# Kernel tuning notes

Hardware: AMD Instinct MI355X
Metric: run time of the kernel (lower is better)

The kernel has to match this reference:

```python
import jax, jax.numpy as jnp
import numpy as np

B, L, HS = 32, 128, 512
P, M = 12, 1024
V, D = 50000, 128
P_TOTAL = 16
CHAR_LEN, CHAR_V = 16, 100
PRI_POS = (0, 1, 2, 3)  # privacy POS tags
TEMP = 1.0              # eval-mode temperature


def setup_inputs() -> dict:
    key = jax.random.key(0)
    ks = jax.random.split(key, 16)
    return {
        "ctx": jax.random.normal(ks[0], (B, L, HS), jnp.float32),
        "dec_W": jax.random.normal(ks[1], (P, HS, M), jnp.float32) * 0.05,
        "dec_b": jax.random.normal(ks[2], (P, M), jnp.float32) * 0.05,
        "psr_weight": jax.random.normal(ks[3], (V, D), jnp.float32),
        "atk_weight": jax.random.normal(ks[4], (V, D), jnp.float32),
        "cpy_W1": jax.random.normal(ks[5], (HS, 64), jnp.float32) * 0.05,
        "cpy_b1": jax.random.normal(ks[6], (64,), jnp.float32) * 0.05,
        "cpy_W2": jax.random.normal(ks[7], (64, 2), jnp.float32) * 0.05,
        "cpy_b2": jax.random.normal(ks[8], (2,), jnp.float32) * 0.05,
        "inp_word": jax.random.randint(ks[9], (B, L), 0, V),
        "inp_pos": jax.random.randint(ks[10], (B, L), 0, P_TOTAL),
        "inp_mask": jnp.ones((B, L), jnp.int32),
        "words": jax.random.randint(ks[11], (P, M), 0, V),
        "lut": jax.random.randint(ks[12], (V, CHAR_LEN), 0, CHAR_V),
    }


def _gumbel_softmax_hard(logits, key, t):
    # hard (straight-through) gumbel-softmax; forward value is one-hot
    u = jax.random.uniform(key, logits.shape, logits.dtype, 1e-6, 1.0 - 1e-6)
    g = -jnp.log(-jnp.log(u))
    y = jax.nn.softmax((logits + g) / t, axis=-1)
    idx = jnp.argmax(y, axis=-1)
    y_hard = jax.nn.one_hot(idx, logits.shape[-1], dtype=y.dtype)
    return y_hard + y - jax.lax.stop_gradient(y), idx


def reference(ctx, dec_W, dec_b, psr_weight, atk_weight,
              cpy_W1, cpy_b1, cpy_W2, cpy_b2,
              inp_word, inp_pos, inp_mask, words, lut):
    bs, ls = inp_word.shape
    N = bs * ls
    gkey = jax.random.key(42)

    ctx_f = ctx.reshape(N, -1)                      # [N, HS]
    pos_f = inp_pos.reshape(N)
    word_f = inp_word.reshape(N)

    ori_psr = psr_weight[word_f]                    # [N, D] gather
    ori_atk = atk_weight[word_f]
    obf_word = word_f
    obf_psr = ori_psr
    obf_atk = ori_atk
    obf_mask = jnp.zeros((N,), bool)
    pri_mask = jnp.zeros((N,), bool)
    entropy = jnp.float32(0.0)

    for p in range(P):  # small fixed set of POS tags (structurally distinct decoders)
        m = pos_f == p                              # [N] routing mask
        obf_mask = obf_mask | m
        if p in PRI_POS:
            pri_mask = pri_mask | m
        cnt = jnp.sum(m.astype(jnp.int32))
        logp = jax.nn.log_softmax(ctx_f @ dec_W[p] + dec_b[p], axis=-1)  # [N, M]
        ent_elem = -logp * jnp.exp(logp)
        ent_p = jnp.sum(jnp.where(m[:, None], ent_elem, 0.0)) / jnp.maximum(cnt * M, 1).astype(jnp.float32)
        entropy = entropy + jnp.where(cnt > 0, ent_p, 0.0)
        spt, idx = _gumbel_softmax_hard(logp, jax.random.fold_in(gkey, p), TEMP)
        spt_word = words[p][idx]                    # map local id -> vocab id
        obf_word = jnp.where(m, spt_word, obf_word)
        psr_p = spt @ psr_weight[words[p]]          # [N, D], per-POS sub-table
        atk_p = spt @ atk_weight[words[p]]
        obf_psr = jnp.where(m[:, None], psr_p, obf_psr)
        obf_atk = jnp.where(m[:, None], atk_p, obf_atk)

    # copy classifier
    h = jax.nn.relu(ctx_f @ cpy_W1 + cpy_b1)
    pcpy = jax.nn.log_softmax(h @ cpy_W2 + cpy_b2, axis=-1)  # [N, 2]
    # do_not_copy_pri: force pcpy to [0, 1] on privacy tokens
    pcpy = jnp.where(pri_mask[:, None], jnp.array([0.0, 1.0], pcpy.dtype), pcpy)

    cpy, _ = _gumbel_softmax_hard(pcpy, jax.random.fold_in(gkey, 999), TEMP)  # [N, 2]
    mask_f = inp_mask.reshape(N).astype(bool)
    cpy_mask = (cpy[:, 0] == 1.0) & mask_f

    noroot = inp_mask.astype(bool).at[:, 0].set(False).reshape(N)
    nr_cnt = jnp.maximum(jnp.sum(noroot.astype(jnp.int32)), 1).astype(jnp.float32)
    logp2 = jax.nn.log_softmax(pcpy, axis=-1)       # F.cross_entropy applies log_softmax again
    cpy_loss = -jnp.sum(jnp.where(noroot, logp2[:, 1], 0.0)) / nr_cnt  # cpy_penalty = 1.0 (applied twice)

    # use_copy: blend original vs obfuscated via (hard) copy gate
    c0, c1 = cpy[:, 0:1], cpy[:, 1:2]
    psr_out = (ori_psr * c0 + obf_psr * c1).reshape(bs, ls, -1)
    atk_out = (ori_atk * c0 + obf_atk * c1).reshape(bs, ls, -1)
    obf_mask = obf_mask & ~cpy_mask
    out_word = (word_f.astype(jnp.float32) * cpy[:, 0]
                + obf_word.astype(jnp.float32) * cpy[:, 1]).astype(jnp.int32).reshape(bs, ls)

    obf_char = lut[out_word]                        # [B, L, CHAR_LEN]
    ent_loss = -entropy  # ent_penalty = 1.0

    return (out_word, obf_char, psr_out, atk_out,
            obf_mask.reshape(bs, ls), cpy_mask.reshape(bs, ls),
            pri_mask.reshape(bs, ls), cpy_loss, ent_loss)
```

## Files before the change

kernel.cpp:

```cpp
#include <hip/hip_runtime.h>
#include <math.h>

#define BB 32
#define LL 128
#define HSZ 512
#define PP 12
#define MM 1024
#define VV 50000
#define DD 128
#define CLEN 16
#define NTOT 4096
#define LISTCAP 512

#define RT 64
#define CT 64
#define BK3 32
#define CPB 16

#define OFF_WORD  0
#define OFF_CHAR  4096
#define OFF_PSR   69632
#define OFF_ATK   593920
#define OFF_OBFM  1118208
#define OFF_CPYM  1122304
#define OFF_PRIM  1126400
#define OFF_CLOSS 1130496
#define OFF_ELOSS 1130497

#define WS_SC_OFF     6656
#define WS_LOGITS_OFF 16384

__device__ __forceinline__ float EXP32(float x){ return (float)exp((double)x); }
__device__ __forceinline__ float LOG32(float x){ return (float)log((double)x); }

__device__ __forceinline__ unsigned rotl32(unsigned x, int r){ return (x<<r)|(x>>(32-r)); }
__device__ __forceinline__ void tf2x32(unsigned k0, unsigned k1, unsigned x0, unsigned x1,
                                       unsigned &o0, unsigned &o1){
  unsigned ks2 = k0 ^ k1 ^ 0x1BD11BDAu;
  x0 += k0; x1 += k1;
  x0+=x1; x1=rotl32(x1,13); x1^=x0;
  x0+=x1; x1=rotl32(x1,15); x1^=x0;
  x0+=x1; x1=rotl32(x1,26); x1^=x0;
  x0+=x1; x1=rotl32(x1, 6); x1^=x0;
  x0+=k1; x1+=ks2+1u;
  x0+=x1; x1=rotl32(x1,17); x1^=x0;
  x0+=x1; x1=rotl32(x1,29); x1^=x0;
  x0+=x1; x1=rotl32(x1,16); x1^=x0;
  x0+=x1; x1=rotl32(x1,24); x1^=x0;
  x0+=ks2; x1+=k0+2u;
  x0+=x1; x1=rotl32(x1,13); x1^=x0;
  x0+=x1; x1=rotl32(x1,15); x1^=x0;
  x0+=x1; x1=rotl32(x1,26); x1^=x0;
  x0+=x1; x1=rotl32(x1, 6); x1^=x0;
  x0+=k0; x1+=k1+3u;
  x0+=x1; x1=rotl32(x1,17); x1^=x0;
  x0+=x1; x1=rotl32(x1,29); x1^=x0;
  x0+=x1; x1=rotl32(x1,16); x1^=x0;
  x0+=x1; x1=rotl32(x1,24); x1^=x0;
  x0+=k1; x1+=ks2+4u;
  x0+=x1; x1=rotl32(x1,13); x1^=x0;
  x0+=x1; x1=rotl32(x1,15); x1^=x0;
  x0+=x1; x1=rotl32(x1,26); x1^=x0;
  x0+=x1; x1=rotl32(x1, 6); x1^=x0;
  x0+=ks2; x1+=k0+5u;
  o0=x0; o1=x1;
}

__device__ __forceinline__ unsigned tf_bits32(unsigned k0, unsigned k1, unsigned e){
  unsigned o0, o1; tf2x32(k0, k1, 0u, e, o0, o1); return o0 ^ o1;
}

__device__ __forceinline__ float bits_to_unif(unsigned bits){
  const float lo = 1e-6f;
  const float hi = (float)(1.0 - 1e-6);
  const float span = hi - lo;
  unsigned fb = (bits >> 9) | 0x3f800000u;
  float f = __fsub_rn(__uint_as_float(fb), 1.0f);
  float r = __fadd_rn(__fmul_rn(f, span), lo);
  return fmaxf(lo, r);
}

__device__ __forceinline__ float gumbel_exact(unsigned bits){
  float u = bits_to_unif(bits);
  float v = -LOG32(u);
  return -LOG32(v);
}
__device__ __forceinline__ float gumbel_fast(unsigned bits){
  float u = bits_to_unif(bits);
  float v = -logf(u);
  return -logf(v);
}

__device__ __forceinline__ void gate_chain(int n, int pos, int msk,
                                           float p0f, float p1f,
                                           const float* __restrict__ cb2,
                                           float* __restrict__ sc0,
                                           float* __restrict__ sc1,
                                           float* __restrict__ closs)
{
  const bool ispri = (pos < 4);
  float pc0 = __fadd_rn(p0f, cb2[0]);
  float pc1 = __fadd_rn(p1f, cb2[1]);
  float m2  = fmaxf(pc0, pc1);
  float s0  = __fsub_rn(pc0, m2), s1 = __fsub_rn(pc1, m2);
  float se  = __fadd_rn(EXP32(s0), EXP32(s1));
  float lse = LOG32(se);
  float q0  = __fsub_rn(s0, lse), q1 = __fsub_rn(s1, lse);
  if (ispri){ q0 = 0.0f; q1 = 1.0f; }

  unsigned k90, k91; tf2x32(0u, 42u, 0u, 999u, k90, k91);
  float g0 = gumbel_exact(tf_bits32(k90, k91, (unsigned)(2*n)));
  float g1 = gumbel_exact(tf_bits32(k90, k91, (unsigned)(2*n + 1)));

  float x0 = __fadd_rn(q0, g0), x1 = __fadd_rn(q1, g1);
  float mmv = fmaxf(x0, x1);
  float ex0 = EXP32(__fsub_rn(x0, mmv));
  float ex1 = EXP32(__fsub_rn(x1, mmv));
  float ssum = __fadd_rn(ex0, ex1);
  float y0 = __fdiv_rn(ex0, ssum), y1 = __fdiv_rn(ex1, ssum);
  int   idx2 = (y1 > y0) ? 1 : 0;
  float ysel = idx2 ? y1 : y0;
  float c    = __fsub_rn(__fadd_rn(1.0f, ysel), ysel);
  *sc0 = (idx2 == 0) ? c : 0.0f;
  *sc1 = (idx2 == 1) ? c : 0.0f;

  float m3 = fmaxf(q0, q1);
  float t0 = __fsub_rn(q0, m3), t1 = __fsub_rn(q1, m3);
  float se2 = __fadd_rn(EXP32(t0), EXP32(t1));
  float l21 = __fsub_rn(t1, LOG32(se2));
  if (msk != 0 && (n & (LL-1)) != 0) atomicAdd(closs, l21);
}

__global__ __launch_bounds__(256)
void cpy_build_kernel(const float* __restrict__ ctx, const float* __restrict__ cW1,
                      const float* __restrict__ cb1, const float* __restrict__ cW2,
                      const float* __restrict__ cb2, const int* __restrict__ inp_pos,
                      const int* __restrict__ inp_mask, int* __restrict__ cntg,
                      int* __restrict__ rowlist, float* __restrict__ scbuf,
                      float* __restrict__ ws)
{
  const int n0 = blockIdx.x * CPB;
  const int t = threadIdx.x;

  if (t < CPB){
    int n = n0 + t;
    int p = inp_pos[n];
    if (p < PP){
      int slot = atomicAdd(&cntg[p], 1);
      if (slot < LISTCAP) rowlist[p*LISTCAP + slot] = n;
    }
  }

  __shared__ float W1s[64][68];
  __shared__ float Cs[CPB][68];

  const int r  = t >> 4;
  const int og = (t & 15) * 4;
  double acc[4] = {0.0, 0.0, 0.0, 0.0};

  for (int k0 = 0; k0 < HSZ; k0 += 64){
    #pragma unroll
    for (int i = 0; i < 4; ++i){
      int s = t + i*256;
      int kk = s >> 4, q = s & 15;
      float4 v = *(const float4*)(cW1 + (size_t)(k0+kk)*64 + q*4);
      *(float4*)&W1s[kk][q*4] = v;
    }
    {
      int rr = t >> 4, q = t & 15;
      float4 v = *(const float4*)(ctx + (size_t)(n0+rr)*HSZ + k0 + q*4);
      *(float4*)&Cs[rr][q*4] = v;
    }
    __syncthreads();
    #pragma unroll 4
    for (int kk = 0; kk < 64; ++kk){
      double c = (double)Cs[r][kk];
      acc[0] += c * (double)W1s[kk][og+0];
      acc[1] += c * (double)W1s[kk][og+1];
      acc[2] += c * (double)W1s[kk][og+2];
      acc[3] += c * (double)W1s[kk][og+3];
    }
    __syncthreads();
  }

  double p0 = 0.0, p1 = 0.0;
  #pragma unroll
  for (int j = 0; j < 4; ++j){
    float hv = __fadd_rn((float)acc[j], cb1[og+j]);
    hv = hv > 0.f ? hv : 0.f;
    double hd = (double)hv;
    p0 += hd * (double)cW2[2*(og+j)+0];
    p1 += hd * (double)cW2[2*(og+j)+1];
  }
  #pragma unroll
  for (int off = 1; off < 16; off <<= 1){
    p0 += __shfl_xor(p0, off);
    p1 += __shfl_xor(p1, off);
  }

  if ((t & 15) == 0){
    const int n = n0 + r;
    float c0v, c1v;
    gate_chain(n, inp_pos[n], inp_mask[n], (float)p0, (float)p1, cb2,
               &c0v, &c1v, ws + 12);
    scbuf[2*n + 0] = c0v;
    scbuf[2*n + 1] = c1v;
  }
}

__global__ __launch_bounds__(256)
void gemm_kernel(const float* __restrict__ ctx, const float* __restrict__ dec_W,
                 const int* __restrict__ cntg, const int* __restrict__ rowlist,
                 float* __restrict__ logits)
{
  const int p  = blockIdx.z;
  const int c0 = blockIdx.x * CT;
  const int r0 = blockIdx.y * RT;
  const int cnt0 = cntg[p];
  const int cnt  = cnt0 < LISTCAP ? cnt0 : LISTCAP;
  if (r0 >= cnt) return;
  const int t = threadIdx.x;

  __shared__ float AsT[BK3][RT+4];
  __shared__ float Bs[BK3][CT+4];
  __shared__ int   rid_s[RT];

  if (t < RT){
    int rr = r0 + t;
    rid_s[t] = rowlist[p*LISTCAP + (rr < cnt ? rr : cnt-1)];
  }
  __syncthreads();

  const int tr = t >> 4, tc = t & 15;
  const int srow = t & 63;
  const int sq   = t >> 6;
  const float* arow = ctx + (size_t)rid_s[srow] * HSZ;

  double acc[4][4];
  #pragma unroll
  for (int i = 0; i < 4; ++i)
    #pragma unroll
    for (int j = 0; j < 4; ++j) acc[i][j] = 0.0;

  const float* Wp = dec_W + (size_t)p * HSZ * MM;

  for (int k0 = 0; k0 < HSZ; k0 += BK3){
    #pragma unroll
    for (int i = 0; i < 2; ++i){
      int kq = sq + i*4;
      float4 v = *(const float4*)(arow + k0 + kq*4);
      AsT[kq*4+0][srow] = v.x;
      AsT[kq*4+1][srow] = v.y;
      AsT[kq*4+2][srow] = v.z;
      AsT[kq*4+3][srow] = v.w;
    }
    #pragma unroll
    for (int i = 0; i < 2; ++i){
      int s = t + i*256;
      int kk = s >> 4, q = s & 15;
      float4 v = *(const float4*)(Wp + (size_t)(k0+kk)*MM + c0 + q*4);
      *(float4*)&Bs[kk][q*4] = v;
    }
    __syncthreads();
    #pragma unroll 4
    for (int kk = 0; kk < BK3; ++kk){
      float4 af = *(const float4*)&AsT[kk][tr*4];
      float4 bf = *(const float4*)&Bs[kk][tc*4];
      double b0=(double)bf.x, b1=(double)bf.y, b2=(double)bf.z, b3=(double)bf.w;
      double a0=(double)af.x, a1=(double)af.y, a2=(double)af.z, a3=(double)af.w;
      acc[0][0]+=a0*b0; acc[0][1]+=a0*b1; acc[0][2]+=a0*b2; acc[0][3]+=a0*b3;
      acc[1][0]+=a1*b0; acc[1][1]+=a1*b1; acc[1][2]+=a1*b2; acc[1][3]+=a1*b3;
      acc[2][0]+=a2*b0; acc[2][1]+=a2*b1; acc[2][2]+=a2*b2; acc[2][3]+=a2*b3;
      acc[3][0]+=a3*b0; acc[3][1]+=a3*b1; acc[3][2]+=a3*b2; acc[3][3]+=a3*b3;
    }
    __syncthreads();
  }

  #pragma unroll
  for (int i = 0; i < 4; ++i){
    int rr = r0 + tr*4 + i;
    if (rr < cnt){
      int rg = rid_s[tr*4 + i];
      float4 o;
      o.x=(float)acc[i][0]; o.y=(float)acc[i][1]; o.z=(float)acc[i][2]; o.w=(float)acc[i][3];
      *(float4*)(logits + (size_t)rg*MM + c0 + tc*4) = o;
    }
  }
}

__global__ __launch_bounds__(256)
void finalize_kernel(const float* __restrict__ dec_b,
                     const float* __restrict__ psr_w, const float* __restrict__ atk_w,
                     const int* __restrict__ inp_word, const int* __restrict__ inp_pos,
                     const int* __restrict__ inp_mask, const int* __restrict__ words,
                     const int* __restrict__ lut, const float* __restrict__ logitsbuf,
                     const float* __restrict__ scbuf,
                     float* __restrict__ out, float* __restrict__ ws)
{
  const int wid = threadIdx.x >> 6, lane = threadIdx.x & 63;
  const int n = blockIdx.x * 4 + wid;

  const int  pos   = inp_pos[n];
  const int  word  = inp_word[n];
  const int  msk   = inp_mask[n];
  const bool isobf = (pos < PP);
  const bool ispri = (pos < 4);
  const float c0 = scbuf[2*n + 0];
  const float c1 = scbuf[2*n + 1];

  int bi = 0;
  if (isobf){
    float l[16];
    float lm = -3.4e38f;
    #pragma unroll
    for (int it = 0; it < 4; ++it){
      int m = it*256 + lane*4;
      float4 lg = *(const float4*)(logitsbuf + (size_t)n*MM + m);
      float4 bq = *(const float4*)(dec_b + (size_t)pos*MM + m);
      l[it*4+0] = __fadd_rn(lg.x, bq.x);
      l[it*4+1] = __fadd_rn(lg.y, bq.y);
      l[it*4+2] = __fadd_rn(lg.z, bq.z);
      l[it*4+3] = __fadd_rn(lg.w, bq.w);
      lm = fmaxf(lm, fmaxf(fmaxf(l[it*4+0], l[it*4+1]), fmaxf(l[it*4+2], l[it*4+3])));
    }
    #pragma unroll
    for (int off = 32; off > 0; off >>= 1) lm = fmaxf(lm, __shfl_xor(lm, off));
    const float xmax = lm;

    float e[16];
    double ds = 0.0;
    #pragma unroll
    for (int j = 0; j < 16; ++j){
      e[j] = expf(__fsub_rn(l[j], xmax));
      ds += (double)e[j];
    }
    #pragma unroll
    for (int off = 32; off > 0; off >>= 1) ds += __shfl_xor(ds, off);
    const double se = ds;
    const float lse = logf((float)se);
    const double inv_se = 1.0 / se;

    unsigned kp0, kp1; tf2x32(0u, 42u, 0u, (unsigned)pos, kp0, kp1);
    float best = -3.4e38f; double es = 0.0;
    #pragma unroll
    for (int it = 0; it < 4; ++it){
      #pragma unroll
      for (int j = 0; j < 4; ++j){
        int m = it*256 + lane*4 + j;
        float sh = __fsub_rn(l[it*4+j], xmax);
        float lp = __fsub_rn(sh, lse);
        es += (double)(-lp) * ((double)e[it*4+j] * inv_se);
        float g = gumbel_fast(tf_bits32(kp0, kp1, (unsigned)(n*MM + m)));
        float sv = __fadd_rn(lp, g);
        if (sv > best){ best = sv; bi = m; }
      }
    }
    #pragma unroll
    for (int off = 32; off > 0; off >>= 1){
      float ov = __shfl_xor(best, off);
      int   oi = __shfl_xor(bi,   off);
      if (ov > best || (ov == best && oi < bi)){ best = ov; bi = oi; }
      es += __shfl_xor(es, off);
    }
    if (lane == 0) atomicAdd(ws + pos, (float)es);
  }

  const int obf_word = isobf ? words[pos*MM + bi] : word;
  float of = __fadd_rn(__fmul_rn((float)word, c0), __fmul_rn((float)obf_word, c1));
  int ow = (int)of;
  if (lane == 0){
    out[OFF_WORD + n] = (float)ow;
    bool cpym = (c0 == 1.0f) && (msk != 0);
    out[OFF_CPYM + n] = cpym ? 1.f : 0.f;
    out[OFF_OBFM + n] = (isobf && !cpym) ? 1.f : 0.f;
    out[OFF_PRIM + n] = ispri ? 1.f : 0.f;
  }
  if (lane < CLEN)
    out[OFF_CHAR + (size_t)n*CLEN + lane] = (float)lut[(size_t)ow*CLEN + lane];
  #pragma unroll
  for (int rep = 0; rep < 2; ++rep){
    int j = lane + rep*64;
    float po = psr_w[(size_t)word*DD + j];
    float pb = isobf ? psr_w[(size_t)obf_word*DD + j] : po;
    out[OFF_PSR + (size_t)n*DD + j] = __fadd_rn(__fmul_rn(po, c0), __fmul_rn(pb, c1));
    float ao = atk_w[(size_t)word*DD + j];
    float ab = isobf ? atk_w[(size_t)obf_word*DD + j] : ao;
    out[OFF_ATK + (size_t)n*DD + j] = __fadd_rn(__fmul_rn(ao, c0), __fmul_rn(ab, c1));
  }
}

__global__ __launch_bounds__(256)
void fin_kernel(const int* __restrict__ inp_pos, const int* __restrict__ inp_mask,
                const float* __restrict__ ws, float* __restrict__ out)
{
  __shared__ int cnt[PP];
  __shared__ int nr;
  int t = threadIdx.x;
  if (t < PP) cnt[t] = 0;
  if (t == 0) nr = 0;
  __syncthreads();
  int ln = 0;
  for (int n = t; n < NTOT; n += 256){
    int p = inp_pos[n];
    if (p < PP) atomicAdd(&cnt[p], 1);
    if (inp_mask[n] != 0 && (n & (LL-1)) != 0) ln++;
  }
  atomicAdd(&nr, ln);
  __syncthreads();
  if (t == 0){
    float ent = 0.f;
    for (int p = 0; p < PP; ++p){
      int c = cnt[p];
      if (c > 0){
        int denom = c * MM; if (denom < 1) denom = 1;
        ent = __fadd_rn(ent, __fdiv_rn(ws[p], (float)denom));
      }
    }
    out[OFF_ELOSS] = -ent;
    int nrc = nr; if (nrc < 1) nrc = 1;
    out[OFF_CLOSS] = -__fdiv_rn(ws[12], (float)nrc);
  }
}

__global__ __launch_bounds__(256)
void row_kernel_mono(const float* __restrict__ ctx, const float* __restrict__ dec_W,
                const float* __restrict__ dec_b, const float* __restrict__ psr_w,
                const float* __restrict__ atk_w, const float* __restrict__ cW1,
                const float* __restrict__ cb1, const float* __restrict__ cW2,
                const float* __restrict__ cb2, const int* __restrict__ inp_word,
                const int* __restrict__ inp_pos, const int* __restrict__ inp_mask,
                const int* __restrict__ words, const int* __restrict__ lut,
                float* __restrict__ out, float* __restrict__ ws)
{
  const int n = blockIdx.x;
  const int t = threadIdx.x;

  __shared__ float  ctx_s[HSZ];
  __shared__ float  logit_s[MM];
  __shared__ float  h_s[64];
  __shared__ double redd[256];
  __shared__ float  redf[256];
  __shared__ int    redi[256];
  __shared__ float  sc[2];
  __shared__ int    si[1];

  for (int k = t; k < HSZ; k += 256) ctx_s[k] = ctx[(size_t)n*HSZ + k];
  __syncthreads();

  const int  pos   = inp_pos[n];
  const int  word  = inp_word[n];
  const int  msk   = inp_mask[n];
  const bool isobf = (pos < PP);
  const bool ispri = (pos < 4);

  if (t < 64){
    double acc = 0.0;
    for (int k = 0; k < HSZ; ++k) acc += (double)ctx_s[k] * (double)cW1[k*64 + t];
    float hv = __fadd_rn((float)acc, cb1[t]);
    h_s[t] = hv > 0.f ? hv : 0.f;
  }
  __syncthreads();

  if (t == 0){
    double a0 = 0.0, a1 = 0.0;
    for (int k = 0; k < 64; ++k){
      double hv = (double)h_s[k];
      a0 += hv * (double)cW2[k*2 + 0];
      a1 += hv * (double)cW2[k*2 + 1];
    }
    float c0v, c1v;
    gate_chain(n, pos, msk, (float)a0, (float)a1, cb2, &c0v, &c1v, ws + 12);
    sc[0] = c0v; sc[1] = c1v;
  }

  if (isobf){
    const float4* W4 = (const float4*)(dec_W + (size_t)pos * HSZ * MM);
    double a0=0.0, a1=0.0, a2=0.0, a3=0.0;
    for (int k = 0; k < HSZ; ++k){
      double c = (double)ctx_s[k];
      float4 w = W4[(size_t)k*256 + t];
      a0 += c*(double)w.x; a1 += c*(double)w.y; a2 += c*(double)w.z; a3 += c*(double)w.w;
    }
    const float* bp = dec_b + (size_t)pos * MM;
    const int m0 = 4*t;
    logit_s[m0+0] = __fadd_rn((float)a0, bp[m0+0]);
    logit_s[m0+1] = __fadd_rn((float)a1, bp[m0+1]);
    logit_s[m0+2] = __fadd_rn((float)a2, bp[m0+2]);
    logit_s[m0+3] = __fadd_rn((float)a3, bp[m0+3]);
    __syncthreads();

    float lm = logit_s[m0];
    lm = fmaxf(lm, logit_s[m0+1]); lm = fmaxf(lm, logit_s[m0+2]); lm = fmaxf(lm, logit_s[m0+3]);
    redf[t] = lm; __syncthreads();
    for (int s = 128; s > 0; s >>= 1){ if (t < s) redf[t] = fmaxf(redf[t], redf[t+s]); __syncthreads(); }
    const float xmax = redf[0];
    __syncthreads();

    double dsm = 0.0;
    for (int j = 0; j < 4; ++j)
      dsm += (double)EXP32(__fsub_rn(logit_s[m0+j], xmax));
    redd[t] = dsm; __syncthreads();
    for (int s = 128; s > 0; s >>= 1){ if (t < s) redd[t] += redd[t+s]; __syncthreads(); }
    const float lse = LOG32((float)redd[0]);
    __syncthreads();

    unsigned kp0, kp1; tf2x32(0u, 42u, 0u, (unsigned)pos, kp0, kp1);
    float best = -3.4e38f; int bi = 0; double es = 0.0;
    for (int j = 0; j < 4; ++j){
      int m = m0 + j;
      float sh = __fsub_rn(logit_s[m], xmax);
      float lp = __fsub_rn(sh, lse);
      float ex = EXP32(lp);
      es += (double)__fmul_rn(-lp, ex);
      float g = gumbel_exact(tf_bits32(kp0, kp1, (unsigned)(n*MM + m)));
      float sv = __fadd_rn(lp, g);
      if (sv > best){ best = sv; bi = m; }
    }
    redf[t] = best; redi[t] = bi; redd[t] = es; __syncthreads();
    for (int s = 128; s > 0; s >>= 1){
      if (t < s){
        float v2 = redf[t+s]; int i2 = redi[t+s];
        if (v2 > redf[t] || (v2 == redf[t] && i2 < redi[t])){ redf[t] = v2; redi[t] = i2; }
        redd[t] += redd[t+s];
      }
      __syncthreads();
    }
    if (t == 0){ si[0] = redi[0]; atomicAdd(ws + pos, (float)redd[0]); }
    __syncthreads();
  } else {
    __syncthreads();
  }

  const int   idx = isobf ? si[0] : 0;
  const float c0 = sc[0], c1 = sc[1];
  const int   obf_word = isobf ? words[pos*MM + idx] : word;

  if (t == 0){
    float of = __fadd_rn(__fmul_rn((float)word, c0), __fmul_rn((float)obf_word, c1));
    int ow = (int)of;
    out[OFF_WORD + n] = (float)ow;
    bool cpym = (c0 == 1.0f) && (msk != 0);
    out[OFF_CPYM + n] = cpym ? 1.f : 0.f;
    out[OFF_OBFM + n] = (isobf && !cpym) ? 1.f : 0.f;
    out[OFF_PRIM + n] = ispri ? 1.f : 0.f;
    #pragma unroll
    for (int j = 0; j < CLEN; ++j)
      out[OFF_CHAR + (size_t)n*CLEN + j] = (float)lut[(size_t)ow*CLEN + j];
  }
  if (t < DD){
    float po = psr_w[(size_t)word*DD + t];
    float pb = isobf ? psr_w[(size_t)obf_word*DD + t] : po;
    out[OFF_PSR + (size_t)n*DD + t] = __fadd_rn(__fmul_rn(po, c0), __fmul_rn(pb, c1));
    float ao = atk_w[(size_t)word*DD + t];
    float ab = isobf ? atk_w[(size_t)obf_word*DD + t] : ao;
    out[OFF_ATK + (size_t)n*DD + t] = __fadd_rn(__fmul_rn(ao, c0), __fmul_rn(ab, c1));
  }
}

extern "C" void kernel_launch(void* const* d_in, const int* in_sizes, int n_in,
                              void* d_out, int out_size, void* d_ws, size_t ws_size,
                              hipStream_t stream)
{
  const float* ctx      = (const float*)d_in[0];
  const float* dec_W    = (const float*)d_in[1];
  const float* dec_b    = (const float*)d_in[2];
  const float* psr_w    = (const float*)d_in[3];
  const float* atk_w    = (const float*)d_in[4];
  const float* cW1      = (const float*)d_in[5];
  const float* cb1      = (const float*)d_in[6];
  const float* cW2      = (const float*)d_in[7];
  const float* cb2      = (const float*)d_in[8];
  const int*   inp_word = (const int*)d_in[9];
  const int*   inp_pos  = (const int*)d_in[10];
  const int*   inp_mask = (const int*)d_in[11];
  const int*   words    = (const int*)d_in[12];
  const int*   lut      = (const int*)d_in[13];
  float* out = (float*)d_out;
  float* ws  = (float*)d_ws;

  const size_t need = ((size_t)WS_LOGITS_OFF + (size_t)NTOT*MM) * 4;

  hipMemsetAsync(ws, 0, 512, stream);

  if (ws_size >= need){
    int*   cntg      = (int*)ws + 16;
    int*   rowlist   = (int*)ws + 64;
    float* scbuf     = ws + WS_SC_OFF;
    float* logitsbuf = ws + WS_LOGITS_OFF;
    cpy_build_kernel<<<NTOT/CPB, 256, 0, stream>>>(ctx, cW1, cb1, cW2, cb2,
                                                   inp_pos, inp_mask, cntg, rowlist,
                                                   scbuf, ws);
    gemm_kernel<<<dim3(MM/CT, LISTCAP/RT, PP), 256, 0, stream>>>(ctx, dec_W, cntg,
                                                                 rowlist, logitsbuf);
    finalize_kernel<<<NTOT/4, 256, 0, stream>>>(dec_b, psr_w, atk_w,
                                                inp_word, inp_pos, inp_mask, words, lut,
                                                logitsbuf, scbuf, out, ws);
  } else {
    row_kernel_mono<<<NTOT, 256, 0, stream>>>(ctx, dec_W, dec_b, psr_w, atk_w,
                                              cW1, cb1, cW2, cb2,
                                              inp_word, inp_pos, inp_mask, words, lut,
                                              out, ws);
  }
  fin_kernel<<<1, 256, 0, stream>>>(inp_pos, inp_mask, ws, out);
}
```

Before: 384.3 us.

## Split GEMM K dimension across two thread groups per block with shared-memory reduction

```diff
diff --git a/kernel.cpp b/kernel.cpp
--- a/kernel.cpp
+++ b/kernel.cpp
@@ -12,9 +12,9 @@
 #define NTOT 4096
 #define LISTCAP 512
 
-#define RT 64
-#define CT 64
-#define BK3 32
+#define RT6 64
+#define CT6 64
+#define BK6 32
 #define CPB 16
 
 #define OFF_WORD  0
@@ -208,34 +208,35 @@
   }
 }
 
-__global__ __launch_bounds__(256)
+__global__ __launch_bounds__(512)
 void gemm_kernel(const float* __restrict__ ctx, const float* __restrict__ dec_W,
                  const int* __restrict__ cntg, const int* __restrict__ rowlist,
                  float* __restrict__ logits)
 {
   const int p  = blockIdx.z;
-  const int c0 = blockIdx.x * CT;
-  const int r0 = blockIdx.y * RT;
+  const int c0 = blockIdx.x * CT6;
+  const int r0 = blockIdx.y * RT6;
   const int cnt0 = cntg[p];
   const int cnt  = cnt0 < LISTCAP ? cnt0 : LISTCAP;
   if (r0 >= cnt) return;
   const int t = threadIdx.x;
-
-  __shared__ float AsT[BK3][RT+4];
-  __shared__ float Bs[BK3][CT+4];
-  __shared__ int   rid_s[RT];
-
-  if (t < RT){
+  const int g  = t >> 8;
+  const int tl = t & 255;
+
+  __shared__ double pool_d[4480];
+  float* pool = (float*)pool_d;
+  float* As = pool + g*4480;
+  float* Bs = pool + g*4480 + 2304;
+  double* comb = pool_d;
+  __shared__ int rid_s[RT6];
+
+  if (t < RT6){
     int rr = r0 + t;
     rid_s[t] = rowlist[p*LISTCAP + (rr < cnt ? rr : cnt-1)];
   }
   __syncthreads();
 
-  const int tr = t >> 4, tc = t & 15;
-  const int srow = t & 63;
-  const int sq   = t >> 6;
-  const float* arow = ctx + (size_t)rid_s[srow] * HSZ;
-
+  const int tr = tl >> 4, tc = tl & 15;
   double acc[4][4];
   #pragma unroll
   for (int i = 0; i < 4; ++i)
@@ -244,30 +245,31 @@
 
   const float* Wp = dec_W + (size_t)p * HSZ * MM;
 
-  for (int k0 = 0; k0 < HSZ; k0 += BK3){
+  for (int it = 0; it < 8; ++it){
+    const int kb = g*256 + it*BK6;
     #pragma unroll
     for (int i = 0; i < 2; ++i){
-      int kq = sq + i*4;
-      float4 v = *(const float4*)(arow + k0 + kq*4);
-      AsT[kq*4+0][srow] = v.x;
-      AsT[kq*4+1][srow] = v.y;
-      AsT[kq*4+2][srow] = v.z;
-      AsT[kq*4+3][srow] = v.w;
+      int s = tl + i*256;
+      int rr = s >> 3, q = s & 7;
+      float4 v = *(const float4*)(ctx + (size_t)rid_s[rr]*HSZ + kb + q*4);
+      *(float4*)&As[rr*36 + q*4] = v;
     }
     #pragma unroll
     for (int i = 0; i < 2; ++i){
-      int s = t + i*256;
+      int s = tl + i*256;
       int kk = s >> 4, q = s & 15;
-      float4 v = *(const float4*)(Wp + (size_t)(k0+kk)*MM + c0 + q*4);
-      *(float4*)&Bs[kk][q*4] = v;
+      float4 v = *(const float4*)(Wp + (size_t)(kb+kk)*MM + c0 + q*4);
+      *(float4*)&Bs[kk*68 + q*4] = v;
     }
     __syncthreads();
     #pragma unroll 4
-    for (int kk = 0; kk < BK3; ++kk){
-      float4 af = *(const float4*)&AsT[kk][tr*4];
-      float4 bf = *(const float4*)&Bs[kk][tc*4];
+    for (int kk = 0; kk < BK6; ++kk){
+      float4 bf = *(const float4*)&Bs[kk*68 + tc*4];
       double b0=(double)bf.x, b1=(double)bf.y, b2=(double)bf.z, b3=(double)bf.w;
-      double a0=(double)af.x, a1=(double)af.y, a2=(double)af.z, a3=(double)af.w;
+      double a0 = (double)As[(tr*4+0)*36 + kk];
+      double a1 = (double)As[(tr*4+1)*36 + kk];
+      double a2 = (double)As[(tr*4+2)*36 + kk];
+      double a3 = (double)As[(tr*4+3)*36 + kk];
       acc[0][0]+=a0*b0; acc[0][1]+=a0*b1; acc[0][2]+=a0*b2; acc[0][3]+=a0*b3;
       acc[1][0]+=a1*b0; acc[1][1]+=a1*b1; acc[1][2]+=a1*b2; acc[1][3]+=a1*b3;
       acc[2][0]+=a2*b0; acc[2][1]+=a2*b1; acc[2][2]+=a2*b2; acc[2][3]+=a2*b3;
@@ -276,14 +278,27 @@
     __syncthreads();
   }
 
-  #pragma unroll
-  for (int i = 0; i < 4; ++i){
-    int rr = r0 + tr*4 + i;
-    if (rr < cnt){
-      int rg = rid_s[tr*4 + i];
-      float4 o;
-      o.x=(float)acc[i][0]; o.y=(float)acc[i][1]; o.z=(float)acc[i][2]; o.w=(float)acc[i][3];
-      *(float4*)(logits + (size_t)rg*MM + c0 + tc*4) = o;
+  if (g == 1){
+    #pragma unroll
+    for (int i = 0; i < 4; ++i)
+      #pragma unroll
+      for (int j = 0; j < 4; ++j)
+        comb[(size_t)(tr*4+i)*64 + tc*4 + j] = acc[i][j];
+  }
+  __syncthreads();
+  if (g == 0){
+    #pragma unroll
+    for (int i = 0; i < 4; ++i){
+      int rr = r0 + tr*4 + i;
+      if (rr < cnt){
+        int rg = rid_s[tr*4 + i];
+        float4 o;
+        o.x = (float)(acc[i][0] + comb[(size_t)(tr*4+i)*64 + tc*4 + 0]);
+        o.y = (float)(acc[i][1] + comb[(size_t)(tr*4+i)*64 + tc*4 + 1]);
+        o.z = (float)(acc[i][2] + comb[(size_t)(tr*4+i)*64 + tc*4 + 2]);
+        o.w = (float)(acc[i][3] + comb[(size_t)(tr*4+i)*64 + tc*4 + 3]);
+        *(float4*)(logits + (size_t)rg*MM + c0 + tc*4) = o;
+      }
     }
   }
 }
@@ -590,8 +605,8 @@
     cpy_build_kernel<<<NTOT/CPB, 256, 0, stream>>>(ctx, cW1, cb1, cW2, cb2,
                                                    inp_pos, inp_mask, cntg, rowlist,
                                                    scbuf, ws);
-    gemm_kernel<<<dim3(MM/CT, LISTCAP/RT, PP), 256, 0, stream>>>(ctx, dec_W, cntg,
-                                                                 rowlist, logitsbuf);
+    gemm_kernel<<<dim3(MM/CT6, LISTCAP/RT6, PP), 512, 0, stream>>>(ctx, dec_W, cntg,
+                                                                   rowlist, logitsbuf);
     finalize_kernel<<<NTOT/4, 256, 0, stream>>>(dec_b, psr_w, atk_w,
                                                 inp_word, inp_pos, inp_mask, words, lut,
                                                 logitsbuf, scbuf, out, ws);
```

Result: faster. 335.0 us (-12.8%).
